# Optimization experiments

Measured on AMD Instinct MI355X. Metric: run time of the kernel, lower is better.

The kernel has to match this reference:

```python
import jax, jax.numpy as jnp
import numpy as np

B, T, V, H = 256, 512, 64, 256
IN = 2 * V + 1  # values + masks + delta_t = 129


def setup_inputs() -> dict:
    key = jax.random.key(0)
    ks = jax.random.split(key, 8)
    # sorted positive times with some entries zeroed (ragged padding -> t_exist False)
    t = jnp.sort(jax.random.uniform(ks[0], (B, T)), axis=1)
    keep = jax.random.uniform(ks[1], (B, T)) < 0.9
    times_in = jnp.where(keep, t, 0.0).astype(jnp.float32)
    data_in = jax.random.normal(ks[2], (B, T, V), dtype=jnp.float32)
    mask_in = (jax.random.uniform(ks[3], (B, T, V)) < 0.8).astype(jnp.float32)
    s = 1.0 / np.sqrt(H).astype(np.float32)
    W_ih = jax.random.uniform(ks[4], (3 * H, IN), minval=-s, maxval=s, dtype=jnp.float32)
    W_hh = jax.random.uniform(ks[5], (3 * H, H), minval=-s, maxval=s, dtype=jnp.float32)
    b_ih = jax.random.uniform(ks[6], (3 * H,), minval=-s, maxval=s, dtype=jnp.float32)
    b_hh = jax.random.uniform(ks[7], (3 * H,), minval=-s, maxval=s, dtype=jnp.float32)
    return {"times_in": times_in, "data_in": data_in, "mask_in": mask_in,
            "W_ih": W_ih, "W_hh": W_hh, "b_ih": b_ih, "b_hh": b_hh}


def reference(times_in, data_in, mask_in, W_ih, W_hh, b_ih, b_hh):
    b = times_in.shape[0]
    # delta_ts: times[:,1:] - times[:,:-1], padded with zero at the end
    delta = jnp.concatenate(
        [times_in[:, 1:] - times_in[:, :-1],
         jnp.zeros((b, 1), times_in.dtype)], axis=1)  # [B,T]
    # input_series = cat(values, masks, delta_t) -> [B,T,2V+1]
    x = jnp.concatenate([data_in, mask_in, delta[..., None]], axis=-1)
    t_exist = times_in > 0  # [B,T]
    h0 = jnp.zeros((b, W_hh.shape[1]), x.dtype)

    xs = (jnp.swapaxes(x, 0, 1), jnp.swapaxes(t_exist, 0, 1))  # time-major

    def step(h, inp):
        xt, m = inp  # xt: [B,IN], m: [B]
        gx = xt @ W_ih.T + b_ih  # [B,3H]
        gh = h @ W_hh.T + b_hh   # [B,3H]
        xr, xz, xn = jnp.split(gx, 3, axis=-1)
        hr, hz, hn = jnp.split(gh, 3, axis=-1)
        r = jax.nn.sigmoid(xr + hr)
        z = jax.nn.sigmoid(xz + hz)
        n = jnp.tanh(xn + r * hn)
        h_new = (1.0 - z) * n + z * h
        h = jnp.where(m[:, None], h_new, h)  # masked state carry
        return h, None

    h_final, _ = jax.lax.scan(step, h0, xs)
    return h_final
```

## Files before the change

### kernel.cpp

```cpp
#include <hip/hip_runtime.h>

#define Bn 256
#define Tn 512
#define Vn 64
#define Hn 256
#define INn 129
#define Cc 8
#define NCH (Tn / Cc)
#define WU 68
#define WSZ (768 * WU)
#define GX_OFF (262144)
#define GX_BYTES ((size_t)Bn * Tn * 768 * 2)
#define AST 168
#define CST 264

typedef __fp16 half2_t __attribute__((ext_vector_type(2)));
typedef __fp16 half8_t __attribute__((ext_vector_type(8)));
typedef float f32x4 __attribute__((ext_vector_type(4)));

static __device__ __forceinline__ unsigned int cvt2(float a, float b) {
  return __builtin_bit_cast(unsigned int, __builtin_amdgcn_cvt_pkrtz(a, b));
}

static __device__ __forceinline__ float dot2(unsigned int w, unsigned int x, float acc) {
#if __has_builtin(__builtin_amdgcn_fdot2)
  return __builtin_amdgcn_fdot2(__builtin_bit_cast(half2_t, w),
                                __builtin_bit_cast(half2_t, x), acc, false);
#else
  half2_t a = __builtin_bit_cast(half2_t, w);
  half2_t b = __builtin_bit_cast(half2_t, x);
  return acc + (float)a.x * (float)b.x + (float)a.y * (float)b.y;
#endif
}

static __device__ __forceinline__ float dot2a(unsigned int w, unsigned int x, float acc) {
  asm("v_dot2_f32_f16 %0, %1, %2, %0" : "+v"(acc) : "v"(w), "v"(x));
  return acc;
}

static __device__ __forceinline__ float pair_sum(float v) {
#if __has_builtin(__builtin_amdgcn_update_dpp)
  int x = __builtin_amdgcn_update_dpp(0, __builtin_bit_cast(int, v), 0xB1, 0xF, 0xF, true);
  return v + __builtin_bit_cast(float, x);
#else
  int j = __builtin_amdgcn_ds_swizzle(__builtin_bit_cast(int, v), 0x041F);
  return v + __builtin_bit_cast(float, j);
#endif
}

static __device__ __forceinline__ float fast_exp2(float x) {
#if __has_builtin(__builtin_amdgcn_exp2f)
  return __builtin_amdgcn_exp2f(x);
#else
  return exp2f(x);
#endif
}
static __device__ __forceinline__ float fast_rcp(float x) {
#if __has_builtin(__builtin_amdgcn_rcpf)
  return __builtin_amdgcn_rcpf(x);
#else
  return 1.f / x;
#endif
}
static __device__ __forceinline__ float sigmoid_f(float x) {
  return fast_rcp(1.f + fast_exp2(-1.44269504f * x));
}
static __device__ __forceinline__ float tanh_f(float x) {
  return 1.f - 2.f * fast_rcp(1.f + fast_exp2(2.88539008f * x));
}

__global__ void convert_wih(const float* __restrict__ W_ih, unsigned int* __restrict__ w16) {
  int idx = blockIdx.x * 256 + threadIdx.x;
  if (idx >= WSZ) return;
  int j = idx / WU, c = idx - j * WU;
  int col = 2 * c;
  float f0 = (col < INn) ? W_ih[(size_t)j * INn + col] : 0.f;
  float f1 = (col + 1 < INn) ? W_ih[(size_t)j * INn + col + 1] : 0.f;
  w16[idx] = cvt2(f0, f1);
}

__global__ __launch_bounds__(256, 4)
void gx_gemm(const float* __restrict__ times_in, const float* __restrict__ data_in,
             const float* __restrict__ mask_in, const unsigned int* __restrict__ w16,
             const float* __restrict__ b_ih, const float* __restrict__ b_hh,
             __fp16* __restrict__ gx) {
  __shared__ __align__(16) char raw[64 * CST * 2];
  __fp16* xa = (__fp16*)raw;
  __fp16* ct = (__fp16*)raw;

  const int tid = threadIdx.x;
  const int bt = blockIdx.x;
  const int b = bt >> 3, tc = bt & 7;
  const int t0 = tc * 64;
  const int n0 = blockIdx.y * 256;

  {
    int r = tid >> 2, s = tid & 3;
    const float* src = (s < 2)
        ? data_in + ((size_t)b * Tn + t0 + r) * Vn + s * 32
        : mask_in + ((size_t)b * Tn + t0 + r) * Vn + (s - 2) * 32;
    unsigned int* dst = (unsigned int*)(xa + r * AST) + s * 16;
#pragma unroll
    for (int i = 0; i < 8; ++i) {
      float4 v = ((const float4*)src)[i];
      dst[2 * i] = cvt2(v.x, v.y);
      dst[2 * i + 1] = cvt2(v.z, v.w);
    }
  }
  if (tid < 64) {
    int g = t0 + tid;
    float tcur = times_in[(size_t)b * Tn + g];
    float d = (g < Tn - 1) ? times_in[(size_t)b * Tn + g + 1] - tcur : 0.f;
    unsigned int* p = (unsigned int*)(xa + tid * AST + 128);
    p[0] = cvt2(d, 0.f);
#pragma unroll
    for (int i = 1; i < 20; ++i) p[i] = 0u;
  }
  __syncthreads();

  const int w = tid >> 6, lane = tid & 63;
  const int m = lane & 15, q = lane >> 4;
  const int nw = n0 + w * 64;

  f32x4 acc[4][4];
#pragma unroll
  for (int i = 0; i < 4; ++i)
#pragma unroll
    for (int j = 0; j < 4; ++j) acc[i][j] = f32x4{0.f, 0.f, 0.f, 0.f};

#pragma unroll
  for (int kt = 0; kt < 5; ++kt) {
    const int k0 = kt * 32 + q * 8;
    half8_t bf[4], af[4];
#pragma unroll
    for (int nt = 0; nt < 4; ++nt) {
      int n = nw + nt * 16 + m;
      uint4 bv = *(const uint4*)(w16 + (size_t)n * WU + (k0 >> 1));
      bf[nt] = __builtin_bit_cast(half8_t, bv);
    }
#pragma unroll
    for (int mt = 0; mt < 4; ++mt) {
      uint4 av = *(const uint4*)(xa + (mt * 16 + m) * AST + k0);
      af[mt] = __builtin_bit_cast(half8_t, av);
    }
#pragma unroll
    for (int mt = 0; mt < 4; ++mt)
#pragma unroll
      for (int nt = 0; nt < 4; ++nt)
        acc[mt][nt] = __builtin_amdgcn_mfma_f32_16x16x32_f16(af[mt], bf[nt], acc[mt][nt], 0, 0, 0);
  }

  float bias[4];
#pragma unroll
  for (int nt = 0; nt < 4; ++nt) {
    int n = nw + nt * 16 + m;
    bias[nt] = b_ih[n] + ((n < 512) ? b_hh[n] : 0.f);
  }

  __syncthreads();
#pragma unroll
  for (int mt = 0; mt < 4; ++mt)
#pragma unroll
    for (int nt = 0; nt < 4; ++nt)
#pragma unroll
      for (int r = 0; r < 4; ++r)
        ct[(mt * 16 + q * 4 + r) * CST + w * 64 + nt * 16 + m] =
            (__fp16)(acc[mt][nt][r] + bias[nt]);
  __syncthreads();

  {
    const int tt = tid >> 2, qq = tid & 3;
    const uint4* src = (const uint4*)(ct + tt * CST) + qq * 8;
    uint4* dst = (uint4*)(gx + ((size_t)b * Tn + t0 + tt) * 768 + n0) + qq * 8;
#pragma unroll
    for (int i = 0; i < 8; ++i) dst[i] = src[i];
  }
}

__global__ __launch_bounds__(512, 1)
void gru_scan8(const float* __restrict__ times_in, const float* __restrict__ W_hh,
               const float* __restrict__ b_hh, const __fp16* __restrict__ gx,
               float* __restrict__ out) {
  __shared__ __align__(16) __fp16 h_buf[2 * Hn];
  __shared__ short act[Tn];
  __shared__ int wave_cnt[8];
  __shared__ int nact_s;

  const int tid = threadIdx.x;
  const int b = blockIdx.x;
  const int jg = tid >> 1;
  const int ks = tid & 1;
  const int lane = tid & 63;
  const int wv = tid >> 6;

  {
    float tv = times_in[(size_t)b * Tn + tid];
    bool on = tv > 0.f;
    unsigned long long mask = __ballot(on);
    int within = __popcll(mask & ((1ull << lane) - 1ull));
    if (lane == 0) wave_cnt[wv] = __popcll(mask);
    __syncthreads();
    int off = 0;
#pragma unroll
    for (int i = 0; i < 8; ++i) off += (i < wv) ? wave_cnt[i] : 0;
    if (on) act[off + within] = (short)tid;
    if (tid == 0) {
      int n = 0;
#pragma unroll
      for (int i = 0; i < 8; ++i) n += wave_cnt[i];
      nact_s = n;
    }
  }

  unsigned int whr[64], whz[64], whn[64];
  {
    const float* w0 = W_hh + (size_t)jg * Hn + ks * 128;
    const float* w1 = W_hh + (size_t)(jg + 256) * Hn + ks * 128;
    const float* w2 = W_hh + (size_t)(jg + 512) * Hn + ks * 128;
#pragma unroll
    for (int c = 0; c < 64; ++c) {
      whr[c] = cvt2(w0[2 * c], w0[2 * c + 1]);
      whz[c] = cvt2(w1[2 * c], w1[2 * c + 1]);
      whn[c] = cvt2(w2[2 * c], w2[2 * c + 1]);
    }
  }
  const float bhn = b_hh[jg + 512];

  h_buf[tid] = (__fp16)0.f;
  __syncthreads();

  const int nact = nact_s;
  const __fp16* gxb = gx + (size_t)b * Tn * 768;
  float hcur = 0.f;
  int cur = 0;

  if (nact > 0) {
    int t0i = act[0];
    float gr = (float)gxb[(size_t)t0i * 768 + jg];
    float gz = (float)gxb[(size_t)t0i * 768 + 256 + jg];
    float gn = (float)gxb[(size_t)t0i * 768 + 512 + jg];

#pragma unroll 1
    for (int i = 0; i < nact; ++i) {
      const int ni = (i + 1 < nact) ? (i + 1) : (nact - 1);
      const int tnx = act[ni];
      const __fp16* p = gxb + (size_t)tnx * 768;
      __fp16 pr = p[jg], pz = p[256 + jg], pn = p[512 + jg];

      const uint4* hb = (const uint4*)(h_buf + cur * Hn) + ks * 16;

      float sr = 0.f, sz = 0.f, shn = 0.f;
      uint4 p0 = hb[0], p1 = hb[1];
#pragma unroll
      for (int cc = 0; cc < 8; ++cc) {
        uint4 q0 = p0, q1 = p1;
        if (cc < 7) { q0 = hb[2 * cc + 2]; q1 = hb[2 * cc + 3]; }
        const int cb = cc * 8;
        sr = dot2a(whr[cb + 0], p0.x, sr);
        sz = dot2a(whz[cb + 0], p0.x, sz);
        shn = dot2a(whn[cb + 0], p0.x, shn);
        sr = dot2a(whr[cb + 1], p0.y, sr);
        sz = dot2a(whz[cb + 1], p0.y, sz);
        shn = dot2a(whn[cb + 1], p0.y, shn);
        sr = dot2a(whr[cb + 2], p0.z, sr);
        sz = dot2a(whz[cb + 2], p0.z, sz);
        shn = dot2a(whn[cb + 2], p0.z, shn);
        sr = dot2a(whr[cb + 3], p0.w, sr);
        sz = dot2a(whz[cb + 3], p0.w, sz);
        shn = dot2a(whn[cb + 3], p0.w, shn);
        sr = dot2a(whr[cb + 4], p1.x, sr);
        sz = dot2a(whz[cb + 4], p1.x, sz);
        shn = dot2a(whn[cb + 4], p1.x, shn);
        sr = dot2a(whr[cb + 5], p1.y, sr);
        sz = dot2a(whz[cb + 5], p1.y, sz);
        shn = dot2a(whn[cb + 5], p1.y, shn);
        sr = dot2a(whr[cb + 6], p1.z, sr);
        sz = dot2a(whz[cb + 6], p1.z, sz);
        shn = dot2a(whn[cb + 6], p1.z, shn);
        sr = dot2a(whr[cb + 7], p1.w, sr);
        sz = dot2a(whz[cb + 7], p1.w, sz);
        shn = dot2a(whn[cb + 7], p1.w, shn);
        p0 = q0; p1 = q1;
      }

      sr = pair_sum(sr);
      sz = pair_sum(sz);
      shn = pair_sum(shn);

      float r = sigmoid_f(gr + sr);
      float z = sigmoid_f(gz + sz);
      float n = tanh_f(gn + r * (shn + bhn));
      hcur = (1.f - z) * n + z * hcur;

      if (ks == 0) h_buf[(cur ^ 1) * Hn + jg] = (__fp16)hcur;
      __syncthreads();
      cur ^= 1;

      gr = (float)pr; gz = (float)pz; gn = (float)pn;
    }
  }

  if (ks == 0) out[(size_t)b * Hn + jg] = hcur;
}

template <bool USE_WS>
static __device__ __forceinline__ void phaseA_pass(int col, const unsigned int* __restrict__ w16,
                                                   const float* __restrict__ W_ih,
                                                   const unsigned int* x_lds, float* a) {
  const uint4* wp = (const uint4*)(w16) + (size_t)col * (WU / 4);
  const float* wf = W_ih + (size_t)col * INn;
#pragma unroll 2
  for (int kp = 0; kp < 8; ++kp) {
    uint4 wa, wb;
    if constexpr (USE_WS) {
      wa = wp[2 * kp];
      wb = wp[2 * kp + 1];
    } else {
      const float* f = wf + 16 * kp;
      wa.x = cvt2(f[0], f[1]);   wa.y = cvt2(f[2], f[3]);
      wa.z = cvt2(f[4], f[5]);   wa.w = cvt2(f[6], f[7]);
      wb.x = cvt2(f[8], f[9]);   wb.y = cvt2(f[10], f[11]);
      wb.z = cvt2(f[12], f[13]); wb.w = cvt2(f[14], f[15]);
    }
#pragma unroll
    for (int t = 0; t < Cc; ++t) {
      const uint4* xp = (const uint4*)&x_lds[t * WU + kp * 8];
      uint4 xa = xp[0], xb = xp[1];
      a[t] = dot2(wa.x, xa.x, a[t]);
      a[t] = dot2(wa.y, xa.y, a[t]);
      a[t] = dot2(wa.z, xa.z, a[t]);
      a[t] = dot2(wa.w, xa.w, a[t]);
      a[t] = dot2(wb.x, xb.x, a[t]);
      a[t] = dot2(wb.y, xb.y, a[t]);
      a[t] = dot2(wb.z, xb.z, a[t]);
      a[t] = dot2(wb.w, xb.w, a[t]);
    }
  }
  uint4 wt;
  if constexpr (USE_WS) {
    wt = wp[16];
  } else {
    wt.x = cvt2(wf[128], 0.f); wt.y = 0u; wt.z = 0u; wt.w = 0u;
  }
#pragma unroll
  for (int t = 0; t < Cc; ++t) {
    uint4 xt = *(const uint4*)&x_lds[t * WU + 64];
    a[t] = dot2(wt.x, xt.x, a[t]);
    a[t] = dot2(wt.y, xt.y, a[t]);
  }
}

template <bool USE_WS>
__global__ __launch_bounds__(512, 2)
void gru_scan_fb(const float* __restrict__ times_in, const float* __restrict__ data_in,
                 const float* __restrict__ mask_in, const unsigned int* __restrict__ w16,
                 const float* __restrict__ W_ih, const float* __restrict__ W_hh,
                 const float* __restrict__ b_ih, const float* __restrict__ b_hh,
                 float* __restrict__ out) {
  __shared__ __align__(16) float gx_lds[Cc * 768];
  __shared__ __align__(16) unsigned int x_lds[Cc * WU];
  __shared__ __align__(16) __fp16 h_buf[2 * Hn];
  __shared__ __align__(16) float t_lds[Tn];

  const int tid = threadIdx.x;
  const int b = blockIdx.x;
  const int jg = tid >> 1;
  const int ks = tid & 1;

  t_lds[tid] = times_in[(size_t)b * Tn + tid];

  unsigned int whr[64], whz[64], whn[64];
  {
    const float* w0 = W_hh + (size_t)jg * Hn + ks * 128;
    const float* w1 = W_hh + (size_t)(jg + 256) * Hn + ks * 128;
    const float* w2 = W_hh + (size_t)(jg + 512) * Hn + ks * 128;
#pragma unroll
    for (int c = 0; c < 64; ++c) {
      whr[c] = cvt2(w0[2 * c], w0[2 * c + 1]);
      whz[c] = cvt2(w1[2 * c], w1[2 * c + 1]);
      whn[c] = cvt2(w2[2 * c], w2[2 * c + 1]);
    }
  }
  const float brh = b_hh[jg];
  const float bzh = b_hh[jg + 256];
  const float bhn = b_hh[jg + 512];
  const float bi1 = b_ih[tid];
  const float bi2 = (tid < 256) ? b_ih[512 + tid] : 0.f;

  h_buf[tid] = (__fp16)0.f;
  __syncthreads();

  float hcur = 0.f;
  int cur = 0;
#pragma unroll 1
  for (int ch = 0; ch < NCH; ++ch) {
    const int t0 = ch * Cc;
    {
      int t = tid >> 6;
      int c = tid & 63;
      const float* src = (c < 32)
          ? data_in + ((size_t)b * Tn + t0 + t) * Vn + 2 * c
          : mask_in + ((size_t)b * Tn + t0 + t) * Vn + 2 * (c - 32);
      float2 v = *(const float2*)src;
      x_lds[t * WU + c] = cvt2(v.x, v.y);
      if (tid < Cc) {
        int g = t0 + tid;
        float d = (g < Tn - 1) ? (t_lds[g + 1] - t_lds[g]) : 0.f;
        uint4 tl;
        tl.x = cvt2(d, 0.f); tl.y = 0u; tl.z = 0u; tl.w = 0u;
        *(uint4*)&x_lds[tid * WU + 64] = tl;
      }
    }
    __syncthreads();
    {
      float a[Cc];
#pragma unroll
      for (int t = 0; t < Cc; ++t) a[t] = bi1;
      phaseA_pass<USE_WS>(tid, w16, W_ih, x_lds, a);
#pragma unroll
      for (int t = 0; t < Cc; ++t) gx_lds[t * 768 + tid] = a[t];
      if (tid < 256) {
#pragma unroll
        for (int t = 0; t < Cc; ++t) a[t] = bi2;
        phaseA_pass<USE_WS>(512 + tid, w16, W_ih, x_lds, a);
#pragma unroll
        for (int t = 0; t < Cc; ++t) gx_lds[t * 768 + 512 + tid] = a[t];
      }
    }
    __syncthreads();
    for (int tt = 0; tt < Cc; ++tt) {
      float sr = 0.f, sz = 0.f, shn = 0.f;
      const uint4* hb = (const uint4*)(h_buf + cur * Hn + ks * 128);
#pragma unroll
      for (int c = 0; c < 16; ++c) {
        uint4 hv = hb[c];
        sr = dot2(whr[4 * c + 0], hv.x, sr);
        sz = dot2(whz[4 * c + 0], hv.x, sz);
        shn = dot2(whn[4 * c + 0], hv.x, shn);
        sr = dot2(whr[4 * c + 1], hv.y, sr);
        sz = dot2(whz[4 * c + 1], hv.y, sz);
        shn = dot2(whn[4 * c + 1], hv.y, shn);
        sr = dot2(whr[4 * c + 2], hv.z, sr);
        sz = dot2(whz[4 * c + 2], hv.z, sz);
        shn = dot2(whn[4 * c + 2], hv.z, shn);
        sr = dot2(whr[4 * c + 3], hv.w, sr);
        sz = dot2(whz[4 * c + 3], hv.w, sz);
        shn = dot2(whn[4 * c + 3], hv.w, shn);
      }
      float gxr = gx_lds[tt * 768 + jg];
      float gxz = gx_lds[tt * 768 + 256 + jg];
      float gxn = gx_lds[tt * 768 + 512 + jg];
      sr = pair_sum(sr);
      sz = pair_sum(sz);
      shn = pair_sum(shn);
      float r = sigmoid_f(gxr + sr + brh);
      float z = sigmoid_f(gxz + sz + bzh);
      float n = tanh_f(gxn + r * (shn + bhn));
      float hN = (1.f - z) * n + z * hcur;
      hcur = (t_lds[t0 + tt] > 0.f) ? hN : hcur;
      if (ks == 0) h_buf[(cur ^ 1) * Hn + jg] = (__fp16)hcur;
      __syncthreads();
      cur ^= 1;
    }
  }
  if (ks == 0) out[(size_t)b * Hn + jg] = hcur;
}

extern "C" void kernel_launch(void* const* d_in, const int* in_sizes, int n_in,
                              void* d_out, int out_size, void* d_ws, size_t ws_size,
                              hipStream_t stream) {
  const float* times_in = (const float*)d_in[0];
  const float* data_in = (const float*)d_in[1];
  const float* mask_in = (const float*)d_in[2];
  const float* W_ih = (const float*)d_in[3];
  const float* W_hh = (const float*)d_in[4];
  const float* b_ih = (const float*)d_in[5];
  const float* b_hh = (const float*)d_in[6];
  float* out = (float*)d_out;

  unsigned int* w16 = (unsigned int*)d_ws;
  __fp16* gx = (__fp16*)((char*)d_ws + GX_OFF);

  if (ws_size >= GX_OFF + GX_BYTES) {
    hipLaunchKernelGGL(convert_wih, dim3((WSZ + 255) / 256), dim3(256), 0, stream, W_ih, w16);
    hipLaunchKernelGGL(gx_gemm, dim3(2048, 3), dim3(256), 0, stream,
                       times_in, data_in, mask_in, w16, b_ih, b_hh, gx);
    hipLaunchKernelGGL(gru_scan8, dim3(Bn), dim3(512), 0, stream,
                       times_in, W_hh, b_hh, gx, out);
  } else if (ws_size >= (size_t)WSZ * 4) {
    hipLaunchKernelGGL(convert_wih, dim3((WSZ + 255) / 256), dim3(256), 0, stream, W_ih, w16);
    hipLaunchKernelGGL((gru_scan_fb<true>), dim3(Bn), dim3(512), 0, stream,
                       times_in, data_in, mask_in, w16, W_ih, W_hh, b_ih, b_hh, out);
  } else {
    hipLaunchKernelGGL((gru_scan_fb<false>), dim3(Bn), dim3(512), 0, stream,
                       times_in, data_in, mask_in, (const unsigned int*)nullptr, W_ih, W_hh,
                       b_ih, b_hh, out);
  }
}
```

Measured before the change: 758.6 us.

## Compute GRU recurrent matvec with MFMA tiles instead of dot2 instructions

The sequential scan kernel now computes the h·W_hhᵀ product with 16x16x32 f16 MFMA instructions. The weights are held as B-fragments in registers, and the hidden state is broadcast across all A rows, so each wave produces 32 hidden units for all three gates. This replaces the per-thread v_dot2 chains and the DPP pair reduction. The time loop is also unrolled by two with the gx loads prefetched, and __syncthreads is replaced by an explicit lgkmcnt wait plus s_barrier. The A-operand work is 16x redundant, so the gain depends on MFMA latency per step being lower than the old VALU dot2 cost.

```diff
diff --git a/kernel.cpp b/kernel.cpp
--- a/kernel.cpp
+++ b/kernel.cpp
@@ -33,11 +33,6 @@
 #endif
 }
 
-static __device__ __forceinline__ float dot2a(unsigned int w, unsigned int x, float acc) {
-  asm("v_dot2_f32_f16 %0, %1, %2, %0" : "+v"(acc) : "v"(w), "v"(x));
-  return acc;
-}
-
 static __device__ __forceinline__ float pair_sum(float v) {
 #if __has_builtin(__builtin_amdgcn_update_dpp)
   int x = __builtin_amdgcn_update_dpp(0, __builtin_bit_cast(int, v), 0xB1, 0xF, 0xF, true);
@@ -68,6 +63,9 @@
 static __device__ __forceinline__ float tanh_f(float x) {
   return 1.f - 2.f * fast_rcp(1.f + fast_exp2(2.88539008f * x));
 }
+static __device__ __forceinline__ float h2f(unsigned short u) {
+  return (float)__builtin_bit_cast(__fp16, u);
+}
 
 __global__ void convert_wih(const float* __restrict__ W_ih, unsigned int* __restrict__ w16) {
   int idx = blockIdx.x * 256 + threadIdx.x;
@@ -177,32 +175,47 @@
   }
 }
 
+struct G6 {
+  unsigned short r0, r1, z0, z1, n0, n1;
+};
+static __device__ __forceinline__ G6 load_gx(const unsigned short* p) {
+  G6 g;
+  g.r0 = p[0];
+  g.r1 = p[16];
+  g.z0 = p[256];
+  g.z1 = p[272];
+  g.n0 = p[512];
+  g.n1 = p[528];
+  return g;
+}
+
 __global__ __launch_bounds__(512, 1)
-void gru_scan8(const float* __restrict__ times_in, const float* __restrict__ W_hh,
-               const float* __restrict__ b_hh, const __fp16* __restrict__ gx,
-               float* __restrict__ out) {
-  __shared__ __align__(16) __fp16 h_buf[2 * Hn];
+void gru_scan_mfma(const float* __restrict__ times_in, const float* __restrict__ W_hh,
+                   const float* __restrict__ b_hh, const __fp16* __restrict__ gx,
+                   float* __restrict__ out) {
+  __shared__ __align__(16) __fp16 hl[2 * Hn];
   __shared__ short act[Tn];
   __shared__ int wave_cnt[8];
   __shared__ int nact_s;
 
   const int tid = threadIdx.x;
   const int b = blockIdx.x;
-  const int jg = tid >> 1;
-  const int ks = tid & 1;
   const int lane = tid & 63;
-  const int wv = tid >> 6;
+  const int w = tid >> 6;
+  const int m = lane & 15;
+  const int q = lane >> 4;
+  const int d0 = w * 32 + m;
 
   {
     float tv = times_in[(size_t)b * Tn + tid];
     bool on = tv > 0.f;
     unsigned long long mask = __ballot(on);
     int within = __popcll(mask & ((1ull << lane) - 1ull));
-    if (lane == 0) wave_cnt[wv] = __popcll(mask);
+    if (lane == 0) wave_cnt[w] = __popcll(mask);
     __syncthreads();
     int off = 0;
 #pragma unroll
-    for (int i = 0; i < 8; ++i) off += (i < wv) ? wave_cnt[i] : 0;
+    for (int i = 0; i < 8; ++i) off += (i < w) ? wave_cnt[i] : 0;
     if (on) act[off + within] = (short)tid;
     if (tid == 0) {
       int n = 0;
@@ -212,95 +225,94 @@
     }
   }
 
-  unsigned int whr[64], whz[64], whn[64];
-  {
-    const float* w0 = W_hh + (size_t)jg * Hn + ks * 128;
-    const float* w1 = W_hh + (size_t)(jg + 256) * Hn + ks * 128;
-    const float* w2 = W_hh + (size_t)(jg + 512) * Hn + ks * 128;
-#pragma unroll
-    for (int c = 0; c < 64; ++c) {
-      whr[c] = cvt2(w0[2 * c], w0[2 * c + 1]);
-      whz[c] = cvt2(w1[2 * c], w1[2 * c + 1]);
-      whn[c] = cvt2(w2[2 * c], w2[2 * c + 1]);
-    }
-  }
-  const float bhn = b_hh[jg + 512];
-
-  h_buf[tid] = (__fp16)0.f;
+  half8_t wb[6][8];
+#pragma unroll
+  for (int g = 0; g < 3; ++g)
+#pragma unroll
+    for (int hf = 0; hf < 2; ++hf) {
+      const float* wr = W_hh + (size_t)(g * 256 + w * 32 + hf * 16 + m) * Hn;
+#pragma unroll
+      for (int kc = 0; kc < 8; ++kc) {
+        const float4 a = *(const float4*)(wr + kc * 32 + q * 8);
+        const float4 c = *(const float4*)(wr + kc * 32 + q * 8 + 4);
+        uint4 u;
+        u.x = cvt2(a.x, a.y);
+        u.y = cvt2(a.z, a.w);
+        u.z = cvt2(c.x, c.y);
+        u.w = cvt2(c.z, c.w);
+        wb[g * 2 + hf][kc] = __builtin_bit_cast(half8_t, u);
+      }
+    }
+  const float bhn0 = b_hh[512 + d0];
+  const float bhn1 = b_hh[512 + d0 + 16];
+
+  hl[tid] = (__fp16)0.f;
   __syncthreads();
 
   const int nact = nact_s;
-  const __fp16* gxb = gx + (size_t)b * Tn * 768;
-  float hcur = 0.f;
+  const unsigned short* gxs = (const unsigned short*)(gx + (size_t)b * Tn * 768) + d0;
+
+  float h0 = 0.f, h1 = 0.f;
   int cur = 0;
 
+  auto step = [&](G6 g) {
+    const uint4* ha = (const uint4*)(hl + cur * Hn);
+    uint4 afu[8];
+#pragma unroll
+    for (int kc = 0; kc < 8; ++kc) afu[kc] = ha[kc * 4 + q];
+
+    f32x4 acc[6];
+#pragma unroll
+    for (int t = 0; t < 6; ++t) acc[t] = f32x4{0.f, 0.f, 0.f, 0.f};
+#pragma unroll
+    for (int kc = 0; kc < 8; ++kc) {
+      half8_t a = __builtin_bit_cast(half8_t, afu[kc]);
+#pragma unroll
+      for (int t = 0; t < 6; ++t)
+        acc[t] = __builtin_amdgcn_mfma_f32_16x16x32_f16(a, wb[t][kc], acc[t], 0, 0, 0);
+    }
+
+    float r0 = sigmoid_f(h2f(g.r0) + acc[0][0]);
+    float r1 = sigmoid_f(h2f(g.r1) + acc[1][0]);
+    float z0 = sigmoid_f(h2f(g.z0) + acc[2][0]);
+    float z1 = sigmoid_f(h2f(g.z1) + acc[3][0]);
+    float n0 = tanh_f(h2f(g.n0) + r0 * (acc[4][0] + bhn0));
+    float n1 = tanh_f(h2f(g.n1) + r1 * (acc[5][0] + bhn1));
+    h0 = z0 * (h0 - n0) + n0;
+    h1 = z1 * (h1 - n1) + n1;
+
+    if (q == 0) {
+      hl[(cur ^ 1) * Hn + d0] = (__fp16)h0;
+      hl[(cur ^ 1) * Hn + d0 + 16] = (__fp16)h1;
+    }
+    asm volatile("s_waitcnt lgkmcnt(0)" ::: "memory");
+    __builtin_amdgcn_s_barrier();
+    __builtin_amdgcn_sched_barrier(0);
+    cur ^= 1;
+  };
+
   if (nact > 0) {
-    int t0i = act[0];
-    float gr = (float)gxb[(size_t)t0i * 768 + jg];
-    float gz = (float)gxb[(size_t)t0i * 768 + 256 + jg];
-    float gn = (float)gxb[(size_t)t0i * 768 + 512 + jg];
-
+    G6 ga = load_gx(gxs + (size_t)act[0] * 768);
+    G6 gb = load_gx(gxs + (size_t)act[(nact > 1) ? 1 : 0] * 768);
+    int i = 0;
 #pragma unroll 1
-    for (int i = 0; i < nact; ++i) {
-      const int ni = (i + 1 < nact) ? (i + 1) : (nact - 1);
-      const int tnx = act[ni];
-      const __fp16* p = gxb + (size_t)tnx * 768;
-      __fp16 pr = p[jg], pz = p[256 + jg], pn = p[512 + jg];
-
-      const uint4* hb = (const uint4*)(h_buf + cur * Hn) + ks * 16;
-
-      float sr = 0.f, sz = 0.f, shn = 0.f;
-      uint4 p0 = hb[0], p1 = hb[1];
-#pragma unroll
-      for (int cc = 0; cc < 8; ++cc) {
-        uint4 q0 = p0, q1 = p1;
-        if (cc < 7) { q0 = hb[2 * cc + 2]; q1 = hb[2 * cc + 3]; }
-        const int cb = cc * 8;
-        sr = dot2a(whr[cb + 0], p0.x, sr);
-        sz = dot2a(whz[cb + 0], p0.x, sz);
-        shn = dot2a(whn[cb + 0], p0.x, shn);
-        sr = dot2a(whr[cb + 1], p0.y, sr);
-        sz = dot2a(whz[cb + 1], p0.y, sz);
-        shn = dot2a(whn[cb + 1], p0.y, shn);
-        sr = dot2a(whr[cb + 2], p0.z, sr);
-        sz = dot2a(whz[cb + 2], p0.z, sz);
-        shn = dot2a(whn[cb + 2], p0.z, shn);
-        sr = dot2a(whr[cb + 3], p0.w, sr);
-        sz = dot2a(whz[cb + 3], p0.w, sz);
-        shn = dot2a(whn[cb + 3], p0.w, shn);
-        sr = dot2a(whr[cb + 4], p1.x, sr);
-        sz = dot2a(whz[cb + 4], p1.x, sz);
-        shn = dot2a(whn[cb + 4], p1.x, shn);
-        sr = dot2a(whr[cb + 5], p1.y, sr);
-        sz = dot2a(whz[cb + 5], p1.y, sz);
-        shn = dot2a(whn[cb + 5], p1.y, shn);
-        sr = dot2a(whr[cb + 6], p1.z, sr);
-        sz = dot2a(whz[cb + 6], p1.z, sz);
-        shn = dot2a(whn[cb + 6], p1.z, shn);
-        sr = dot2a(whr[cb + 7], p1.w, sr);
-        sz = dot2a(whz[cb + 7], p1.w, sz);
-        shn = dot2a(whn[cb + 7], p1.w, shn);
-        p0 = q0; p1 = q1;
-      }
-
-      sr = pair_sum(sr);
-      sz = pair_sum(sz);
-      shn = pair_sum(shn);
-
-      float r = sigmoid_f(gr + sr);
-      float z = sigmoid_f(gz + sz);
-      float n = tanh_f(gn + r * (shn + bhn));
-      hcur = (1.f - z) * n + z * hcur;
-
-      if (ks == 0) h_buf[(cur ^ 1) * Hn + jg] = (__fp16)hcur;
-      __syncthreads();
-      cur ^= 1;
-
-      gr = (float)pr; gz = (float)pz; gn = (float)pn;
-    }
-  }
-
-  if (ks == 0) out[(size_t)b * Hn + jg] = hcur;
+    for (; i + 2 <= nact; i += 2) {
+      const int iA = (i + 2 < nact) ? i + 2 : nact - 1;
+      const int iB = (i + 3 < nact) ? i + 3 : nact - 1;
+      const int tA = act[iA];
+      const int tB = act[iB];
+      step(ga);
+      ga = load_gx(gxs + (size_t)tA * 768);
+      step(gb);
+      gb = load_gx(gxs + (size_t)tB * 768);
+    }
+    if (i < nact) step(ga);
+  }
+
+  if (q == 0) {
+    out[(size_t)b * Hn + d0] = h0;
+    out[(size_t)b * Hn + d0 + 16] = h1;
+  }
 }
 
 template <bool USE_WS>
@@ -485,7 +497,7 @@
     hipLaunchKernelGGL(convert_wih, dim3((WSZ + 255) / 256), dim3(256), 0, stream, W_ih, w16);
     hipLaunchKernelGGL(gx_gemm, dim3(2048, 3), dim3(256), 0, stream,
                        times_in, data_in, mask_in, w16, b_ih, b_hh, gx);
-    hipLaunchKernelGGL(gru_scan8, dim3(Bn), dim3(512), 0, stream,
+    hipLaunchKernelGGL(gru_scan_mfma, dim3(Bn), dim3(512), 0, stream,
                        times_in, W_hh, b_hh, gx, out);
   } else if (ws_size >= (size_t)WSZ * 4) {
     hipLaunchKernelGGL(convert_wih, dim3((WSZ + 255) / 256), dim3(256), 0, stream, W_ih, w16);
```

New measurement: 721.5 us. 4.9% less time.
